# Performance work log

Measured on AMD Instinct MI355X. Metric: run time of the kernel, lower is better.

## Reference

```python
import jax, jax.numpy as jnp
import numpy as np

# Module hyperparameters (init_kwargs): dim=128, res=128, idx=0, split_size=8, num_heads=8
B, RES, DIM, NH = 8, 128, 128, 8
HD = DIM // NH               # head_dim = 16
HSP, WSP = RES, 8            # idx=0 -> H_sp=res, W_sp=split_size
N = HSP * WSP                # tokens per window
SCALE = HD ** -0.5
L = RES * RES


def setup_inputs() -> dict:
    key = jax.random.key(0)
    k1, k2, k3 = jax.random.split(key, 3)
    return {
        "qkv": jax.random.normal(k1, (3, B, L, DIM), dtype=jnp.float32),
        "conv_w": jax.random.normal(k2, (DIM, 1, 3, 3), dtype=jnp.float32) * 0.1,
        "conv_b": jax.random.normal(k3, (DIM,), dtype=jnp.float32) * 0.1,
    }


def _im2cswin(x):
    # x: [B, L, C] -> windows as heads: [B*nW, NH, N, HD]
    x = jnp.transpose(x, (0, 2, 1)).reshape(B, DIM, RES, RES)
    x = x.reshape(B, DIM, RES // HSP, HSP, RES // WSP, WSP)
    x = jnp.transpose(x, (0, 2, 4, 3, 5, 1)).reshape(-1, N, DIM)
    x = x.reshape(-1, N, NH, HD)
    return jnp.transpose(x, (0, 2, 1, 3))


def reference(qkv, conv_w, conv_b):
    q, k, v = qkv[0], qkv[1], qkv[2]
    k = _im2cswin(k)                               # [W, NH, N, HD]
    v = _im2cswin(v)                               # [W, NH, N, HD]

    # q -> per-window image blocks [B*nW, C, H_sp, W_sp]
    qi = jnp.transpose(q, (0, 2, 1)).reshape(B, DIM, RES, RES)
    qi = qi.reshape(B, DIM, RES // HSP, HSP, RES // WSP, WSP)
    qi = jnp.transpose(qi, (0, 2, 4, 1, 3, 5)).reshape(-1, DIM, HSP, WSP)

    # depthwise 3x3 conv LePE
    lepe = jax.lax.conv_general_dilated(
        qi, conv_w, window_strides=(1, 1), padding='SAME',
        feature_group_count=DIM,
        dimension_numbers=('NCHW', 'OIHW', 'NCHW'))
    lepe = lepe + conv_b[None, :, None, None]
    lepe = jnp.transpose(lepe.reshape(-1, NH, HD, N), (0, 1, 3, 2))  # [W, NH, N, HD]
    qh = jnp.transpose(qi.reshape(-1, NH, HD, N), (0, 1, 3, 2))      # [W, NH, N, HD]

    # linear attention: softmax over scaled K^T V (d x d)
    att = jnp.einsum('wnid,wnie->wnde', k, v) * SCALE                # [W, NH, HD, HD]
    att = jax.nn.softmax(att, axis=-1)
    x = jnp.einsum('wnid,wnde->wnie', qh, att) + lepe                # [W, NH, N, HD]

    # windows -> image -> [B, L, C]
    x = jnp.transpose(x, (0, 2, 1, 3)).reshape(-1, N, DIM)
    x = x.reshape(B, RES // HSP, RES // WSP, HSP, WSP, DIM)
    x = jnp.transpose(x, (0, 1, 3, 2, 4, 5)).reshape(B, RES, RES, DIM)
    return x.reshape(B, L, DIM)
```

## Files before the change

### kernel.cpp

```cpp
#include <hip/hip_runtime.h>


static constexpr int BB   = 8;
static constexpr int RES  = 128;
static constexpr int DIM  = 128;
static constexpr int WSP  = 8;
static constexpr int L    = RES * RES;
static constexpr float SCALE = 0.25f;
static constexpr int QROW = 260;
static constexpr int QBUF = 18 * QROW;

#define GLD_LDS16(g, l)                                                        \
  __builtin_amdgcn_global_load_lds(                                            \
      (const __attribute__((address_space(1))) void*)(const void*)(g),         \
      (__attribute__((address_space(3))) void*)(l), 16, 0, 0)

__global__ __launch_bounds__(256, 2) void fused_lepe(
    const float* __restrict__ Qg, const float* __restrict__ Kg,
    const float* __restrict__ Vg, const float* __restrict__ cw,
    const float* __restrict__ cb, float* __restrict__ outp) {
  __shared__ float smem[16896];
  float* const A_sm    = smem + 16384;
  float* const scratch = smem;

  const int b  = blockIdx.x;
  const int w  = b >> 2, g = b & 3;
  const int bi = w >> 4, wb = w & 15;
  const int t  = threadIdx.x;
  const int wave = t >> 6, lane = t & 63;
  const size_t win_base = (size_t)(bi * L + wb * WSP) * DIM;
  const int ch0 = g * 32;

  const int h1 = lane >> 5, dq = (lane >> 3) & 3, ep = lane & 7;
  const int kaddr = h1 * 16 + dq * 4;
  const int vaddr = h1 * 16 + ep * 2;
  const int n0 = wave * 32;

  float a00=0.f,a01=0.f,a10=0.f,a11=0.f,a20=0.f,a21=0.f,a30=0.f,a31=0.f;

  auto stageKV = [&](int tile, int buf) {
    for (int c = wave; c < 32; c += 4) {
      const int mat = c >> 4, rr = c & 15;
      const int r = tile * 16 + rr;
      const float* src = (mat ? Vg : Kg) + win_base +
                         (size_t)r * (RES * DIM) + (lane >> 3) * DIM + ch0 +
                         (lane & 7) * 4;
      float* dst = smem + mat * 8192 + buf * 4096 + rr * 256;
      GLD_LDS16(src, dst);
    }
  };

  stageKV(0, 0);
  __syncthreads();
  for (int tt = 0; tt < 8; ++tt) {
    const int cur = tt & 1;
    if (tt < 7) stageKV(tt + 1, cur ^ 1);
    const float* Kb = smem + cur * 4096;
    const float* Vb = smem + 8192 + cur * 4096;
#pragma unroll 4
    for (int n = n0; n < n0 + 32; ++n) {
      const float4 k4 = *reinterpret_cast<const float4*>(&Kb[n * 32 + kaddr]);
      const float2 v2 = *reinterpret_cast<const float2*>(&Vb[n * 32 + vaddr]);
      a00 += k4.x * v2.x; a01 += k4.x * v2.y;
      a10 += k4.y * v2.x; a11 += k4.y * v2.y;
      a20 += k4.z * v2.x; a21 += k4.z * v2.y;
      a30 += k4.w * v2.x; a31 += k4.w * v2.y;
    }
    __syncthreads();
  }

  auto stageQ = [&](int tile, int buf) {
    const int r0 = tile * 16;
    float* qb = smem + buf * QBUF;
    for (int c = wave; c < 18; c += 4) {
      const int r = r0 - 1 + c;
      float* dst = qb + c * QROW;
      if ((unsigned)r < 128u) {
        const float* src = Qg + win_base + (size_t)r * (RES * DIM) +
                           (lane >> 3) * DIM + ch0 + (lane & 7) * 4;
        GLD_LDS16(src, dst);
      } else {
        *reinterpret_cast<float4*>(dst + lane * 4) =
            make_float4(0.f, 0.f, 0.f, 0.f);
      }
    }
  };

  stageQ(0, 1);
  {
    float* sc = scratch + wave * 512 + lane * 8;
    sc[0]=a00; sc[1]=a01; sc[2]=a10; sc[3]=a11;
    sc[4]=a20; sc[5]=a21; sc[6]=a30; sc[7]=a31;
  }
  __syncthreads();

  {
    const int r = t >> 3, e2 = t & 7;
    const int h = r >> 4, d = r & 15;
    const int f = (h * 32 + (d >> 2) * 8 + e2) * 8 + (d & 3) * 2;
    float v0 = (scratch[f]     + scratch[512 + f]     + scratch[1024 + f]     + scratch[1536 + f]) * SCALE;
    float v1 = (scratch[f + 1] + scratch[512 + f + 1] + scratch[1024 + f + 1] + scratch[1536 + f + 1]) * SCALE;
    float m = fmaxf(v0, v1);
    m = fmaxf(m, __shfl_xor(m, 1));
    m = fmaxf(m, __shfl_xor(m, 2));
    m = fmaxf(m, __shfl_xor(m, 4));
    v0 = __expf(v0 - m); v1 = __expf(v1 - m);
    float ss = v0 + v1;
    ss += __shfl_xor(ss, 1);
    ss += __shfl_xor(ss, 2);
    ss += __shfl_xor(ss, 4);
    const float ri = 1.0f / ss;
    A_sm[r * 16 + e2 * 2 + 0] = v0 * ri;
    A_sm[r * 16 + e2 * 2 + 1] = v1 * ri;
  }
  __syncthreads();

  const int cq   = t & 7;
  const int lr   = (t >> 3) & 15;
  const int half = t >> 7;
  const int hg = cq >> 2, e0 = (cq & 3) * 4;
  const int cg = ch0 + cq * 4;

  float4 Acol[16];
#pragma unroll
  for (int d = 0; d < 16; ++d)
    Acol[d] = *reinterpret_cast<const float4*>(&A_sm[(hg * 16 + d) * 16 + e0]);
  float4 wgt[9];
#pragma unroll
  for (int tap = 0; tap < 9; ++tap) {
    wgt[tap].x = cw[(cg + 0) * 9 + tap];
    wgt[tap].y = cw[(cg + 1) * 9 + tap];
    wgt[tap].z = cw[(cg + 2) * 9 + tap];
    wgt[tap].w = cw[(cg + 3) * 9 + tap];
  }
  const float4 bias = *reinterpret_cast<const float4*>(&cb[cg]);
  const float4 zero4 = make_float4(0.f, 0.f, 0.f, 0.f);

#define ACC(qs, d)                                                             \
  o.x += (qs) * Acol[d].x; o.y += (qs) * Acol[d].y;                            \
  o.z += (qs) * Acol[d].z; o.w += (qs) * Acol[d].w;

  int buf = 1;
  for (int tile = 0; tile < 8; ++tile) {
    if (tile < 7) stageQ(tile + 1, buf ^ 1);
    const float* Qb = smem + buf * QBUF;
    const int r0 = tile * 16;
    const int w0 = half * 4;

    float4 cL[3], cC[3], cR[3];
    auto ldcol = [&](int cidx, float4* dv) {
#pragma unroll
      for (int dy = 0; dy < 3; ++dy)
        dv[dy] = ((unsigned)cidx < 8u)
                     ? *reinterpret_cast<const float4*>(
                           &Qb[(lr + dy) * QROW + cidx * 32 + cq * 4])
                     : zero4;
    };
    ldcol(w0 - 1, cL);
    ldcol(w0, cC);

#pragma unroll
    for (int k = 0; k < 4; ++k) {
      const int wl = w0 + k;
      ldcol(wl + 1, cR);
      float4 o = bias;
#pragma unroll
      for (int dy = 0; dy < 3; ++dy) {
        const int t0 = dy * 3;
        o.x += cL[dy].x * wgt[t0].x + cC[dy].x * wgt[t0+1].x + cR[dy].x * wgt[t0+2].x;
        o.y += cL[dy].y * wgt[t0].y + cC[dy].y * wgt[t0+1].y + cR[dy].y * wgt[t0+2].y;
        o.z += cL[dy].z * wgt[t0].z + cC[dy].z * wgt[t0+1].z + cR[dy].z * wgt[t0+2].z;
        o.w += cL[dy].w * wgt[t0].w + cC[dy].w * wgt[t0+1].w + cR[dy].w * wgt[t0+2].w;
      }
      const float* qr = &Qb[(lr + 1) * QROW + wl * 32 + hg * 16];
      const float4 q0 = *reinterpret_cast<const float4*>(qr + 0);
      const float4 q1 = *reinterpret_cast<const float4*>(qr + 4);
      const float4 q2 = *reinterpret_cast<const float4*>(qr + 8);
      const float4 q3 = *reinterpret_cast<const float4*>(qr + 12);
      ACC(q0.x, 0)  ACC(q0.y, 1)  ACC(q0.z, 2)  ACC(q0.w, 3)
      ACC(q1.x, 4)  ACC(q1.y, 5)  ACC(q1.z, 6)  ACC(q1.w, 7)
      ACC(q2.x, 8)  ACC(q2.y, 9)  ACC(q2.z, 10) ACC(q2.w, 11)
      ACC(q3.x, 12) ACC(q3.y, 13) ACC(q3.z, 14) ACC(q3.w, 15)

      float* dst = outp + win_base + (size_t)(r0 + lr) * (RES * DIM) +
                   wl * DIM + cg;
      *reinterpret_cast<float4*>(dst) = o;

#pragma unroll
      for (int dy = 0; dy < 3; ++dy) { cL[dy] = cC[dy]; cC[dy] = cR[dy]; }
    }
    __syncthreads();
    buf ^= 1;
  }
#undef ACC
}

extern "C" void kernel_launch(void* const* d_in, const int* in_sizes, int n_in,
                              void* d_out, int out_size, void* d_ws,
                              size_t ws_size, hipStream_t stream) {
  const float* qkv = (const float*)d_in[0];
  const float* cw  = (const float*)d_in[1];
  const float* cb  = (const float*)d_in[2];
  const float* Qg = qkv;
  const float* Kg = qkv + (size_t)BB * L * DIM;
  const float* Vg = Kg + (size_t)BB * L * DIM;
  float* outp = (float*)d_out;

  fused_lepe<<<512, 256, 0, stream>>>(Qg, Kg, Vg, cw, cb, outp);
}
```

Measured before the change: 62.59 us.

## Split fused kernel into gram and apply kernels with more blocks

Splits the single fused kernel into two launches. The first computes partial K^T V Gram matrices over half-windows into workspace across 1024 blocks. The second, across 2048 blocks, combines them, applies softmax and computes output plus depthwise conv, reading Q directly from global memory instead of staging halos in LDS. This raises parallelism and occupancy but adds a second launch, a workspace round trip, and redundant global loads for the conv neighbours.

After: 76.21 us. +21.8%, slower.

```diff
diff --git a/kernel.cpp b/kernel.cpp
--- a/kernel.cpp
+++ b/kernel.cpp
@@ -6,59 +6,57 @@
 static constexpr int DIM  = 128;
 static constexpr int WSP  = 8;
 static constexpr int L    = RES * RES;
+static constexpr int ROWSTRIDE = RES * DIM;
 static constexpr float SCALE = 0.25f;
-static constexpr int QROW = 260;
-static constexpr int QBUF = 18 * QROW;
 
 #define GLD_LDS16(g, l)                                                        \
   __builtin_amdgcn_global_load_lds(                                            \
       (const __attribute__((address_space(1))) void*)(const void*)(g),         \
       (__attribute__((address_space(3))) void*)(l), 16, 0, 0)
 
-__global__ __launch_bounds__(256, 2) void fused_lepe(
-    const float* __restrict__ Qg, const float* __restrict__ Kg,
-    const float* __restrict__ Vg, const float* __restrict__ cw,
-    const float* __restrict__ cb, float* __restrict__ outp) {
-  __shared__ float smem[16896];
-  float* const A_sm    = smem + 16384;
-  float* const scratch = smem;
-
-  const int b  = blockIdx.x;
-  const int w  = b >> 2, g = b & 3;
-  const int bi = w >> 4, wb = w & 15;
-  const int t  = threadIdx.x;
+__global__ __launch_bounds__(256, 4) void gram_kernel(
+    const float* __restrict__ Kg, const float* __restrict__ Vg,
+    float* __restrict__ ws) {
+  __shared__ float smem[10240];
+
+  const int b    = blockIdx.x;
+  const int win  = b >> 3;
+  const int hp   = (b >> 1) & 3;
+  const int half = b & 1;
+  const int bi = win >> 4, wb = win & 15;
+  const int t = threadIdx.x;
   const int wave = t >> 6, lane = t & 63;
   const size_t win_base = (size_t)(bi * L + wb * WSP) * DIM;
-  const int ch0 = g * 32;
+  const int ch0 = hp * 32;
+  const int rbase = half * 64;
 
   const int h1 = lane >> 5, dq = (lane >> 3) & 3, ep = lane & 7;
   const int kaddr = h1 * 16 + dq * 4;
   const int vaddr = h1 * 16 + ep * 2;
-  const int n0 = wave * 32;
+  const int n0 = wave * 16;
 
   float a00=0.f,a01=0.f,a10=0.f,a11=0.f,a20=0.f,a21=0.f,a30=0.f,a31=0.f;
 
-  auto stageKV = [&](int tile, int buf) {
-    for (int c = wave; c < 32; c += 4) {
-      const int mat = c >> 4, rr = c & 15;
-      const int r = tile * 16 + rr;
+  auto stage = [&](int tile, int buf) {
+    for (int c = wave; c < 16; c += 4) {
+      const int mat = c >> 3, rr = c & 7;
       const float* src = (mat ? Vg : Kg) + win_base +
-                         (size_t)r * (RES * DIM) + (lane >> 3) * DIM + ch0 +
-                         (lane & 7) * 4;
-      float* dst = smem + mat * 8192 + buf * 4096 + rr * 256;
+                         (size_t)(rbase + tile * 8 + rr) * ROWSTRIDE +
+                         (lane >> 3) * DIM + ch0 + (lane & 7) * 4;
+      float* dst = smem + mat * 4096 + buf * 2048 + rr * 256;
       GLD_LDS16(src, dst);
     }
   };
 
-  stageKV(0, 0);
+  stage(0, 0);
   __syncthreads();
   for (int tt = 0; tt < 8; ++tt) {
     const int cur = tt & 1;
-    if (tt < 7) stageKV(tt + 1, cur ^ 1);
-    const float* Kb = smem + cur * 4096;
-    const float* Vb = smem + 8192 + cur * 4096;
+    if (tt < 7) stage(tt + 1, cur ^ 1);
+    const float* Kb = smem + cur * 2048;
+    const float* Vb = smem + 4096 + cur * 2048;
 #pragma unroll 4
-    for (int n = n0; n < n0 + 32; ++n) {
+    for (int n = n0; n < n0 + 16; ++n) {
       const float4 k4 = *reinterpret_cast<const float4*>(&Kb[n * 32 + kaddr]);
       const float2 v2 = *reinterpret_cast<const float2*>(&Vb[n * 32 + vaddr]);
       a00 += k4.x * v2.x; a01 += k4.x * v2.y;
@@ -69,37 +67,43 @@
     __syncthreads();
   }
 
-  auto stageQ = [&](int tile, int buf) {
-    const int r0 = tile * 16;
-    float* qb = smem + buf * QBUF;
-    for (int c = wave; c < 18; c += 4) {
-      const int r = r0 - 1 + c;
-      float* dst = qb + c * QROW;
-      if ((unsigned)r < 128u) {
-        const float* src = Qg + win_base + (size_t)r * (RES * DIM) +
-                           (lane >> 3) * DIM + ch0 + (lane & 7) * 4;
-        GLD_LDS16(src, dst);
-      } else {
-        *reinterpret_cast<float4*>(dst + lane * 4) =
-            make_float4(0.f, 0.f, 0.f, 0.f);
-      }
-    }
-  };
-
-  stageQ(0, 1);
   {
-    float* sc = scratch + wave * 512 + lane * 8;
-    sc[0]=a00; sc[1]=a01; sc[2]=a10; sc[3]=a11;
-    sc[4]=a20; sc[5]=a21; sc[6]=a30; sc[7]=a31;
+    float* sc = smem + 8192 + wave * 512 + h1 * 256 + ep * 2;
+    *reinterpret_cast<float2*>(&sc[(dq * 4 + 0) * 16]) = make_float2(a00, a01);
+    *reinterpret_cast<float2*>(&sc[(dq * 4 + 1) * 16]) = make_float2(a10, a11);
+    *reinterpret_cast<float2*>(&sc[(dq * 4 + 2) * 16]) = make_float2(a20, a21);
+    *reinterpret_cast<float2*>(&sc[(dq * 4 + 3) * 16]) = make_float2(a30, a31);
   }
   __syncthreads();
 
+  float* wsb = ws + (size_t)b * 512;
+  const float* sc = smem + 8192;
+  for (int i = t; i < 512; i += 256)
+    wsb[i] = sc[i] + sc[512 + i] + sc[1024 + i] + sc[1536 + i];
+}
+
+__global__ __launch_bounds__(256, 3) void apply_kernel(
+    const float* __restrict__ Qg, const float* __restrict__ ws,
+    const float* __restrict__ cw, const float* __restrict__ cb,
+    float* __restrict__ outp) {
+  __shared__ float A_sm[512];
+
+  const int b   = blockIdx.x;
+  const int win = b >> 4;
+  const int hp  = (b >> 2) & 3;
+  const int qr  = b & 3;
+  const int bi = win >> 4, wb = win & 15;
+  const int t = threadIdx.x;
+  const size_t win_base = (size_t)(bi * L + wb * WSP) * DIM;
+  const int ch0 = hp * 32;
+
   {
+    const float* w0 = ws + (size_t)((win * 4 + hp) * 2 + 0) * 512;
+    const float* w1 = ws + (size_t)((win * 4 + hp) * 2 + 1) * 512;
     const int r = t >> 3, e2 = t & 7;
-    const int h = r >> 4, d = r & 15;
-    const int f = (h * 32 + (d >> 2) * 8 + e2) * 8 + (d & 3) * 2;
-    float v0 = (scratch[f]     + scratch[512 + f]     + scratch[1024 + f]     + scratch[1536 + f]) * SCALE;
-    float v1 = (scratch[f + 1] + scratch[512 + f + 1] + scratch[1024 + f + 1] + scratch[1536 + f + 1]) * SCALE;
+    const int idx = r * 16 + e2 * 2;
+    float v0 = (w0[idx]     + w1[idx])     * SCALE;
+    float v1 = (w0[idx + 1] + w1[idx + 1]) * SCALE;
     float m = fmaxf(v0, v1);
     m = fmaxf(m, __shfl_xor(m, 1));
     m = fmaxf(m, __shfl_xor(m, 2));
@@ -110,16 +114,16 @@
     ss += __shfl_xor(ss, 2);
     ss += __shfl_xor(ss, 4);
     const float ri = 1.0f / ss;
-    A_sm[r * 16 + e2 * 2 + 0] = v0 * ri;
-    A_sm[r * 16 + e2 * 2 + 1] = v1 * ri;
+    A_sm[idx]     = v0 * ri;
+    A_sm[idx + 1] = v1 * ri;
   }
   __syncthreads();
 
-  const int cq   = t & 7;
-  const int lr   = (t >> 3) & 15;
-  const int half = t >> 7;
+  const int cq = t & 7;
+  const int lr = t >> 3;
   const int hg = cq >> 2, e0 = (cq & 3) * 4;
   const int cg = ch0 + cq * 4;
+  const int row = qr * 32 + lr;
 
   float4 Acol[16];
 #pragma unroll
@@ -136,61 +140,57 @@
   const float4 bias = *reinterpret_cast<const float4*>(&cb[cg]);
   const float4 zero4 = make_float4(0.f, 0.f, 0.f, 0.f);
 
+  const bool up_ok = (row > 0), dn_ok = (row < 127);
+  const float* qconv = Qg + win_base + (size_t)row * ROWSTRIDE + cg;
+  const float* qhead = Qg + win_base + (size_t)row * ROWSTRIDE + ch0 + hg * 16;
+
+  auto ldcol = [&](int c, float4* dv) {
+    if ((unsigned)c >= 8u) {
+      dv[0] = zero4; dv[1] = zero4; dv[2] = zero4;
+      return;
+    }
+    const float* p = qconv + c * DIM;
+    dv[0] = up_ok ? *reinterpret_cast<const float4*>(p - ROWSTRIDE) : zero4;
+    dv[1] = *reinterpret_cast<const float4*>(p);
+    dv[2] = dn_ok ? *reinterpret_cast<const float4*>(p + ROWSTRIDE) : zero4;
+  };
+
 #define ACC(qs, d)                                                             \
   o.x += (qs) * Acol[d].x; o.y += (qs) * Acol[d].y;                            \
   o.z += (qs) * Acol[d].z; o.w += (qs) * Acol[d].w;
 
-  int buf = 1;
-  for (int tile = 0; tile < 8; ++tile) {
-    if (tile < 7) stageQ(tile + 1, buf ^ 1);
-    const float* Qb = smem + buf * QBUF;
-    const int r0 = tile * 16;
-    const int w0 = half * 4;
-
-    float4 cL[3], cC[3], cR[3];
-    auto ldcol = [&](int cidx, float4* dv) {
-#pragma unroll
-      for (int dy = 0; dy < 3; ++dy)
-        dv[dy] = ((unsigned)cidx < 8u)
-                     ? *reinterpret_cast<const float4*>(
-                           &Qb[(lr + dy) * QROW + cidx * 32 + cq * 4])
-                     : zero4;
-    };
-    ldcol(w0 - 1, cL);
-    ldcol(w0, cC);
-
-#pragma unroll
-    for (int k = 0; k < 4; ++k) {
-      const int wl = w0 + k;
-      ldcol(wl + 1, cR);
-      float4 o = bias;
-#pragma unroll
-      for (int dy = 0; dy < 3; ++dy) {
-        const int t0 = dy * 3;
-        o.x += cL[dy].x * wgt[t0].x + cC[dy].x * wgt[t0+1].x + cR[dy].x * wgt[t0+2].x;
-        o.y += cL[dy].y * wgt[t0].y + cC[dy].y * wgt[t0+1].y + cR[dy].y * wgt[t0+2].y;
-        o.z += cL[dy].z * wgt[t0].z + cC[dy].z * wgt[t0+1].z + cR[dy].z * wgt[t0+2].z;
-        o.w += cL[dy].w * wgt[t0].w + cC[dy].w * wgt[t0+1].w + cR[dy].w * wgt[t0+2].w;
-      }
-      const float* qr = &Qb[(lr + 1) * QROW + wl * 32 + hg * 16];
-      const float4 q0 = *reinterpret_cast<const float4*>(qr + 0);
-      const float4 q1 = *reinterpret_cast<const float4*>(qr + 4);
-      const float4 q2 = *reinterpret_cast<const float4*>(qr + 8);
-      const float4 q3 = *reinterpret_cast<const float4*>(qr + 12);
+  float4 cL[3], cC[3], cR[3];
+  ldcol(-1, cL);
+  ldcol(0, cC);
+
+#pragma unroll
+  for (int wl = 0; wl < 8; ++wl) {
+    ldcol(wl + 1, cR);
+    float4 o = bias;
+#pragma unroll
+    for (int dy = 0; dy < 3; ++dy) {
+      const int t0 = dy * 3;
+      o.x += cL[dy].x * wgt[t0].x + cC[dy].x * wgt[t0+1].x + cR[dy].x * wgt[t0+2].x;
+      o.y += cL[dy].y * wgt[t0].y + cC[dy].y * wgt[t0+1].y + cR[dy].y * wgt[t0+2].y;
+      o.z += cL[dy].z * wgt[t0].z + cC[dy].z * wgt[t0+1].z + cR[dy].z * wgt[t0+2].z;
+      o.w += cL[dy].w * wgt[t0].w + cC[dy].w * wgt[t0+1].w + cR[dy].w * wgt[t0+2].w;
+    }
+    {
+      const float* qh = qhead + wl * DIM;
+      const float4 q0 = *reinterpret_cast<const float4*>(qh + 0);
+      const float4 q1 = *reinterpret_cast<const float4*>(qh + 4);
+      const float4 q2 = *reinterpret_cast<const float4*>(qh + 8);
+      const float4 q3 = *reinterpret_cast<const float4*>(qh + 12);
       ACC(q0.x, 0)  ACC(q0.y, 1)  ACC(q0.z, 2)  ACC(q0.w, 3)
       ACC(q1.x, 4)  ACC(q1.y, 5)  ACC(q1.z, 6)  ACC(q1.w, 7)
       ACC(q2.x, 8)  ACC(q2.y, 9)  ACC(q2.z, 10) ACC(q2.w, 11)
       ACC(q3.x, 12) ACC(q3.y, 13) ACC(q3.z, 14) ACC(q3.w, 15)
-
-      float* dst = outp + win_base + (size_t)(r0 + lr) * (RES * DIM) +
-                   wl * DIM + cg;
-      *reinterpret_cast<float4*>(dst) = o;
-
-#pragma unroll
-      for (int dy = 0; dy < 3; ++dy) { cL[dy] = cC[dy]; cC[dy] = cR[dy]; }
-    }
-    __syncthreads();
-    buf ^= 1;
+    }
+    float* dst = outp + win_base + (size_t)row * ROWSTRIDE + wl * DIM + cg;
+    *reinterpret_cast<float4*>(dst) = o;
+
+#pragma unroll
+    for (int dy = 0; dy < 3; ++dy) { cL[dy] = cC[dy]; cC[dy] = cR[dy]; }
   }
 #undef ACC
 }
@@ -204,7 +204,9 @@
   const float* Qg = qkv;
   const float* Kg = qkv + (size_t)BB * L * DIM;
   const float* Vg = Kg + (size_t)BB * L * DIM;
+  float* ws   = (float*)d_ws;
   float* outp = (float*)d_out;
 
-  fused_lepe<<<512, 256, 0, stream>>>(Qg, Kg, Vg, cw, cb, outp);
+  gram_kernel<<<1024, 256, 0, stream>>>(Kg, Vg, ws);
+  apply_kernel<<<2048, 256, 0, stream>>>(Qg, ws, cw, cb, outp);
 }
```
